# Kernel tuning notes

Measured on AMD Instinct MI355X. Metric: run time of the kernel, lower is better.

The kernel has to match this reference:

```python
import jax, jax.numpy as jnp
import numpy as np

B, T, S, K = 512, 16, 64, 32  # batch, delta_t, num_sensors, num_clusters


def setup_inputs() -> dict:
    key = jax.random.key(0)
    k1, k2, k3 = jax.random.split(key, 3)
    X = jax.random.normal(k1, (B, T, S), dtype=jnp.float32)
    mu = jax.random.normal(k2, (K, S), dtype=jnp.float32)            # cluster means
    A = jax.random.normal(k3, (T, K, S, S), dtype=jnp.float32)       # Toeplitz block generators
    return {"X": X, "mu": mu, "A": A}


def _build_mat(A):
    # A: [T, K, S, S] -> block-Toeplitz mat: [K, T*S, T*S]
    # block(i, j) = A[i-j].T if i >= j else A[j-i]
    T_, K_, S_, _ = A.shape
    idx = jnp.arange(T_)
    diff = idx[:, None] - idx[None, :]                 # [T, T]
    blocks = A[jnp.abs(diff)]                          # [T, T, K, S, S]
    blocks_t = jnp.swapaxes(blocks, -1, -2)
    blocks = jnp.where((diff >= 0)[:, :, None, None, None], blocks_t, blocks)
    # [T, T, K, S, S] -> [K, T, S, T, S] -> [K, T*S, T*S]
    return jnp.transpose(blocks, (2, 0, 3, 1, 4)).reshape(K_, T_ * S_, T_ * S_)


def reference(X, mu, A):
    T_, K_, S_, _ = A.shape
    # dX: [B, K, T, S] -> flatten time*sensor -> [B, K, D]
    dX = (X[:, None, :, :] - mu[None, :, None, :]).reshape(X.shape[0], K_, T_ * S_)
    mat = _build_mat(A)                                # [K, D, D]
    P1 = jnp.einsum('bkd,kde,bke->bk', dX, mat, dX)    # quadratic form
    P2 = jnp.linalg.slogdet(mat)[1]                    # [K] log|det|
    lle = -0.5 * P1 + P2[None, :]
    return jax.nn.softmax(lle, axis=-1)
```

## Files before the change

kernel.cpp:

```cpp
#include <hip/hip_runtime.h>
#include <math.h>

static constexpr int B_ = 512;
static constexpr int T_ = 16;
static constexpr int S_ = 64;
static constexpr int K_ = 32;
static constexpr int N_ = 1024;

__global__ void initk(int* __restrict__ rowmap, float* __restrict__ logdet) {
  int idx = blockIdx.x * 256 + threadIdx.x;
  if (idx < K_ * N_) rowmap[idx] = idx & (N_ - 1);
  if (idx < K_) logdet[idx] = 0.f;
}

__global__ __launch_bounds__(256) void buildM(const float* __restrict__ A, float* __restrict__ M) {
  int k = blockIdx.z, i = blockIdx.y, j = blockIdx.x;
  int d = i - j;
  int ad = d >= 0 ? d : -d;
  const float* Ad = A + ((size_t)(ad * K_ + k) << 12);
  float* out = M + ((size_t)k << 20) + (size_t)(i * 64) * N_ + j * 64;
  int tid = threadIdx.x;
  if (d < 0) {
    for (int x = tid; x < 1024; x += 256) {
      int a = x >> 4, b4 = (x & 15) << 2;
      *(float4*)(out + (size_t)a * N_ + b4) = *(const float4*)(Ad + a * 64 + b4);
    }
  } else {
    __shared__ float ts[64][65];
    for (int x = tid; x < 1024; x += 256) {
      int r = x >> 4, c4 = (x & 15) << 2;
      float4 v = *(const float4*)(Ad + r * 64 + c4);
      ts[c4 + 0][r] = v.x; ts[c4 + 1][r] = v.y; ts[c4 + 2][r] = v.z; ts[c4 + 3][r] = v.w;
    }
    __syncthreads();
    for (int x = tid; x < 1024; x += 256) {
      int a = x >> 4, b4 = (x & 15) << 2;
      float4 v;
      v.x = ts[a][b4 + 0]; v.y = ts[a][b4 + 1]; v.z = ts[a][b4 + 2]; v.w = ts[a][b4 + 3];
      *(float4*)(out + (size_t)a * N_ + b4) = v;
    }
  }
}

__global__ __launch_bounds__(256) void prepk(const float* __restrict__ A, const float* __restrict__ mu,
                                             float* __restrict__ rbuf, float* __restrict__ cterm) {
  int k = blockIdx.x;
  __shared__ float smu[64];
  __shared__ float sp[1024], sq[1024];
  int tid = threadIdx.x;
  if (tid < 64) smu[tid] = mu[k * 64 + tid];
  __syncthreads();
  for (int idx = tid; idx < 1024; idx += 256) {
    int d = idx >> 6, s = idx & 63;
    const float* Ad = A + ((size_t)(d * K_ + k) << 12);
    float ap = 0.f, aq = 0.f;
    for (int s2 = 0; s2 < 64; ++s2) {
      ap += Ad[s * 64 + s2] * smu[s2];
      aq += Ad[s2 * 64 + s] * smu[s2];
    }
    sp[idx] = ap; sq[idx] = aq;
  }
  __syncthreads();
  for (int idx = tid; idx < 1024; idx += 256) {
    int j = idx >> 6, s = idx & 63;
    float acc = 0.5f * (sp[s] + sq[s]);
    for (int d = 1; d < 16; ++d) {
      if (d <= 15 - j) acc += sp[d * 64 + s];
      if (d <= j)      acc += sq[d * 64 + s];
    }
    rbuf[k * 1024 + idx] = acc;
  }
  if (tid < 64) {
    float a = 16.f * sp[tid];
    for (int d = 1; d < 16; ++d) a += 2.f * (float)(16 - d) * sp[d * 64 + tid];
    a *= smu[tid];
    for (int off = 32; off; off >>= 1) a += __shfl_xor(a, off);
    if (tid == 0) cterm[k] = a;
  }
}

__global__ __launch_bounds__(256) void qkern(const float* __restrict__ X, const float* __restrict__ A,
                                             float* __restrict__ Qp) {
  int g = blockIdx.x;
  int btile = blockIdx.y;
  __shared__ float Xs[4][1024];
  __shared__ float Cs[4][4096];
  int tid = threadIdx.x;
  int wave = tid >> 6, lane = tid & 63;
  for (int t = tid; t < 4096; t += 256) {
    int bb = t >> 10, e = t & 1023;
    Xs[bb][e] = X[(size_t)(btile * 4 + bb) * 1024 + e];
  }
  float regQ[4][8];
#pragma unroll
  for (int bb = 0; bb < 4; ++bb)
#pragma unroll
    for (int kk = 0; kk < 8; ++kk) regQ[bb][kk] = 0.f;

  int a0 = (tid >> 4) << 2;
  int v0 = (tid & 15) << 2;
  for (int dd = 0; dd < 4; ++dd) {
    int d = g + (dd << 2);
    __syncthreads();
    for (int bb = 0; bb < 4; ++bb) {
      float4 r0 = {0,0,0,0}, r1 = {0,0,0,0}, r2 = {0,0,0,0}, r3 = {0,0,0,0};
      for (int j = 0; j + d < 16; ++j) {
        const float4 xa = *(const float4*)&Xs[bb][j * 64 + a0];
        const float4 xv = *(const float4*)&Xs[bb][(j + d) * 64 + v0];
        r0.x += xa.x * xv.x; r0.y += xa.x * xv.y; r0.z += xa.x * xv.z; r0.w += xa.x * xv.w;
        r1.x += xa.y * xv.x; r1.y += xa.y * xv.y; r1.z += xa.y * xv.z; r1.w += xa.y * xv.w;
        r2.x += xa.z * xv.x; r2.y += xa.z * xv.y; r2.z += xa.z * xv.z; r2.w += xa.z * xv.w;
        r3.x += xa.w * xv.x; r3.y += xa.w * xv.y; r3.z += xa.w * xv.z; r3.w += xa.w * xv.w;
      }
      *(float4*)&Cs[bb][(a0 + 0) * 64 + v0] = r0;
      *(float4*)&Cs[bb][(a0 + 1) * 64 + v0] = r1;
      *(float4*)&Cs[bb][(a0 + 2) * 64 + v0] = r2;
      *(float4*)&Cs[bb][(a0 + 3) * 64 + v0] = r3;
    }
    __syncthreads();
    float w = (d == 0) ? 1.f : 2.f;
    for (int ch = 0; ch < 16; ++ch) {
      int e4 = (ch * 64 + lane) << 2;
      float4 cv[4];
#pragma unroll
      for (int bb = 0; bb < 4; ++bb) {
        float4 t4 = *(const float4*)&Cs[bb][e4];
        cv[bb].x = w * t4.x; cv[bb].y = w * t4.y; cv[bb].z = w * t4.z; cv[bb].w = w * t4.w;
      }
#pragma unroll
      for (int kk = 0; kk < 8; ++kk) {
        int k = wave + (kk << 2);
        const float4 av = *(const float4*)(A + (((size_t)(d * K_ + k)) << 12) + e4);
#pragma unroll
        for (int bb = 0; bb < 4; ++bb)
          regQ[bb][kk] += av.x * cv[bb].x + av.y * cv[bb].y + av.z * cv[bb].z + av.w * cv[bb].w;
      }
    }
  }
#pragma unroll
  for (int bb = 0; bb < 4; ++bb)
#pragma unroll
    for (int kk = 0; kk < 8; ++kk) {
      float v = regQ[bb][kk];
      for (int off = 32; off; off >>= 1) v += __shfl_xor(v, off);
      regQ[bb][kk] = v;
    }
  if (lane == 0) {
    int b = btile * 4;
#pragma unroll
    for (int bb = 0; bb < 4; ++bb)
#pragma unroll
      for (int kk = 0; kk < 8; ++kk)
        Qp[((size_t)(g * B_ + b + bb) << 5) + (wave + (kk << 2))] = regQ[bb][kk];
  }
}

__global__ __launch_bounds__(1024) void panelk(float* __restrict__ M, int* __restrict__ rowmap,
                                               float* __restrict__ logdet, float* __restrict__ Uws,
                                               int j0) {
  int k = blockIdx.x;
  float* Mk = M + ((size_t)k << 20);
  int* rmk = rowmap + (k << 10);
  int m = N_ - j0;
  int t = threadIdx.x;
  int bdim = blockDim.x;
  int lane = t & 63, wid = t >> 6;
  int nw = (bdim + 63) >> 6;

  __shared__ float bufP[32];
  __shared__ float bufJ[32];
  __shared__ int origP, origJ;
  __shared__ float candv[16];
  __shared__ int candi[16];
  __shared__ int spiv;
  __shared__ float l11s[32 * 33];
  __shared__ int smapU[32];

  float r[32];
  int myorig = -1;
  float mydiag = 1.f;
  bool act = (t < m);
  if (act) {
    myorig = rmk[j0 + t];
    const float* src = Mk + (size_t)myorig * N_ + j0;
#pragma unroll
    for (int c4 = 0; c4 < 8; ++c4) *(float4*)&r[c4 * 4] = *(const float4*)(src + c4 * 4);
  }

#pragma unroll
  for (int jj = 0; jj < 32; ++jj) {
    float bv = (act && t >= jj) ? fabsf(r[jj]) : -1.f;
    int bi = t;
#pragma unroll
    for (int off = 32; off; off >>= 1) {
      float ov = __shfl_xor(bv, off);
      int oi = __shfl_xor(bi, off);
      if (ov > bv) { bv = ov; bi = oi; }
    }
    if (lane == 0) { candv[wid] = bv; candi[wid] = bi; }
    __syncthreads();
    if (t < 64) {
      float cv = (lane < nw) ? candv[lane] : -1.f;
      int ci = (lane < nw) ? candi[lane] : 0;
#pragma unroll
      for (int off = 8; off; off >>= 1) {
        float ov = __shfl_down(cv, off, 16);
        int oi = __shfl_down(ci, off, 16);
        if (ov > cv) { cv = ov; ci = oi; }
      }
      if (lane == 0) spiv = ci;
    }
    __syncthreads();
    int p = spiv;
    if (t == p) {
#pragma unroll
      for (int c4 = 0; c4 < 8; ++c4) *(float4*)&bufP[c4 * 4] = *(const float4*)&r[c4 * 4];
      origP = myorig;
    }
    if (p != jj && t == jj) {
#pragma unroll
      for (int c4 = 0; c4 < 8; ++c4) *(float4*)&bufJ[c4 * 4] = *(const float4*)&r[c4 * 4];
      origJ = myorig;
    }
    __syncthreads();
    float pr[32];
#pragma unroll
    for (int c4 = 0; c4 < 8; ++c4) *(float4*)&pr[c4 * 4] = *(const float4*)&bufP[c4 * 4];
    if (p != jj) {
      if (t == jj) {
#pragma unroll
        for (int c = 0; c < 32; ++c) r[c] = pr[c];
        myorig = origP;
      } else if (t == p) {
#pragma unroll
        for (int c4 = 0; c4 < 8; ++c4) *(float4*)&r[c4 * 4] = *(const float4*)&bufJ[c4 * 4];
        myorig = origJ;
      }
    }
    float pv = pr[jj];
    if (t == jj) mydiag = pv;
    float sinv = 1.0f / pv;
    if (act && t > jj) {
      float mult = r[jj] * sinv;
      r[jj] = mult;
#pragma unroll
      for (int c = jj + 1; c < 32; ++c) r[c] -= mult * pr[c];
    }
  }

  if (t < 32) {
    float lv = logf(fabsf(mydiag));
#pragma unroll
    for (int off = 16; off; off >>= 1) lv += __shfl_down(lv, off, 32);
    if (t == 0) logdet[k] += lv;
  }
  if (t < 32) {
#pragma unroll
    for (int c = 0; c < 32; ++c) l11s[t * 33 + c] = r[c];
    smapU[t] = myorig;
  }
  if (act) {
    float* dst = Mk + (size_t)(j0 + t) * N_ + j0;
#pragma unroll
    for (int c4 = 0; c4 < 8; ++c4) *(float4*)(dst + c4 * 4) = *(const float4*)&r[c4 * 4];
    rmk[j0 + t] = myorig;
  }
  __syncthreads();

  int mprime = m - 32;
  if (t < mprime) {
    int col = j0 + 32 + t;
    float* Uk = Uws + ((size_t)k << 15);
    float u[32];
#pragma unroll
    for (int rr = 0; rr < 32; ++rr) {
      float av = Mk[(size_t)smapU[rr] * N_ + col];
#pragma unroll
      for (int tt = 0; tt < 32; ++tt) { if (tt < rr) av -= l11s[rr * 33 + tt] * u[tt]; }
      u[rr] = av;
      Uk[(rr << 10) + col] = av;
    }
  }
}

__global__ __launch_bounds__(256) void updatek(float* __restrict__ M, const int* __restrict__ rowmap,
                                               const float* __restrict__ Uws, int j0) {
  int k = blockIdx.z;
  int mprime = N_ - j0 - 32;
  int r0 = blockIdx.y << 7;
  int c0 = blockIdx.x << 7;
  float* Mk = M + ((size_t)k << 20);
  const int* rmk = rowmap + (k << 10);
  __shared__ float LtT[32 * 132];
  __shared__ float Ut[32 * 132];
  __shared__ int rowL[128];
  int tid = threadIdx.x;

  if (tid < 128) rowL[tid] = (r0 + tid < mprime) ? rmk[j0 + 32 + r0 + tid] : -1;
  for (int x = tid; x < 1024; x += 256) {
    int rI = x >> 3, q = (x & 7) << 2;
    float4 v = {0.f, 0.f, 0.f, 0.f};
    if (r0 + rI < mprime) v = *(const float4*)(Mk + (size_t)(j0 + 32 + r0 + rI) * N_ + j0 + q);
    LtT[(q + 0) * 132 + rI] = v.x;
    LtT[(q + 1) * 132 + rI] = v.y;
    LtT[(q + 2) * 132 + rI] = v.z;
    LtT[(q + 3) * 132 + rI] = v.w;
  }
  {
    const float* Uk = Uws + ((size_t)k << 15) + j0 + 32 + c0;
    for (int x = tid; x < 1024; x += 256) {
      int rr = x >> 5, c4 = (x & 31) << 2;
      float4 v = {0.f, 0.f, 0.f, 0.f};
      if (c0 + c4 < mprime) v = *(const float4*)(Uk + (rr << 10) + c4);
      *(float4*)&Ut[rr * 132 + c4] = v;
    }
  }
  __syncthreads();

  int tx = tid & 15, ty = tid >> 4;
  int cc = c0 + (tx << 2);

  float4 cur[2][2][4];
#pragma unroll
  for (int ri = 0; ri < 2; ++ri)
#pragma unroll
    for (int r = 0; r < 4; ++r) {
      int lr = (ty << 2) + r + (ri << 6);
      int pr = rowL[lr];
#pragma unroll
      for (int ci = 0; ci < 2; ++ci) {
        int lc = cc + (ci << 6);
        if (pr >= 0 && lc < mprime)
          cur[ri][ci][r] = *(const float4*)(Mk + (size_t)pr * N_ + j0 + 32 + lc);
        else
          cur[ri][ci][r] = make_float4(0.f, 0.f, 0.f, 0.f);
      }
    }

#define FMS4(dst, s, b4) dst.x -= (s) * b4.x; dst.y -= (s) * b4.y; dst.z -= (s) * b4.z; dst.w -= (s) * b4.w;
#pragma unroll 8
  for (int tk = 0; tk < 32; ++tk) {
    float4 aL = *(const float4*)&LtT[tk * 132 + (ty << 2)];
    float4 aH = *(const float4*)&LtT[tk * 132 + (ty << 2) + 64];
    float4 bL = *(const float4*)&Ut[tk * 132 + (tx << 2)];
    float4 bH = *(const float4*)&Ut[tk * 132 + (tx << 2) + 64];
    FMS4(cur[0][0][0], aL.x, bL) FMS4(cur[0][0][1], aL.y, bL) FMS4(cur[0][0][2], aL.z, bL) FMS4(cur[0][0][3], aL.w, bL)
    FMS4(cur[0][1][0], aL.x, bH) FMS4(cur[0][1][1], aL.y, bH) FMS4(cur[0][1][2], aL.z, bH) FMS4(cur[0][1][3], aL.w, bH)
    FMS4(cur[1][0][0], aH.x, bL) FMS4(cur[1][0][1], aH.y, bL) FMS4(cur[1][0][2], aH.z, bL) FMS4(cur[1][0][3], aH.w, bL)
    FMS4(cur[1][1][0], aH.x, bH) FMS4(cur[1][1][1], aH.y, bH) FMS4(cur[1][1][2], aH.z, bH) FMS4(cur[1][1][3], aH.w, bH)
  }
#undef FMS4

#pragma unroll
  for (int ri = 0; ri < 2; ++ri)
#pragma unroll
    for (int r = 0; r < 4; ++r) {
      int lr = (ty << 2) + r + (ri << 6);
      int pr = rowL[lr];
      if (pr < 0) continue;
      float* rowp = Mk + (size_t)pr * N_ + j0 + 32;
#pragma unroll
      for (int ci = 0; ci < 2; ++ci) {
        int lc = cc + (ci << 6);
        if (lc < mprime) *(float4*)(rowp + lc) = cur[ri][ci][r];
      }
    }
}

__global__ __launch_bounds__(256) void finalk(const float* __restrict__ X, const float* __restrict__ rbuf,
                                              const float* __restrict__ cterm, const float* __restrict__ logdet,
                                              const float* __restrict__ Qp, float* __restrict__ out) {
  int b = blockIdx.x;
  __shared__ float Xs[1024];
  __shared__ float lleS[32];
  int tid = threadIdx.x, wave = tid >> 6, lane = tid & 63;
  for (int i = tid; i < 1024; i += 256) Xs[i] = X[(size_t)b * 1024 + i];
  __syncthreads();
#pragma unroll
  for (int kk = 0; kk < 8; ++kk) {
    int k = wave + (kk << 2);
    const float* rk = rbuf + (size_t)k * 1024;
    float acc = 0.f;
#pragma unroll
    for (int ch = 0; ch < 4; ++ch) {
      int e4 = (ch * 64 + lane) << 2;
      const float4 rv = *(const float4*)(rk + e4);
      const float4 xv = *(const float4*)&Xs[e4];
      acc += rv.x * xv.x + rv.y * xv.y + rv.z * xv.z + rv.w * xv.w;
    }
    for (int off = 32; off; off >>= 1) acc += __shfl_xor(acc, off);
    if (lane == 0) {
      float Qv = 0.f;
#pragma unroll
      for (int g = 0; g < 4; ++g) Qv += Qp[((size_t)(g * B_ + b) << 5) + k];
      float P1 = Qv - 2.f * acc + cterm[k];
      lleS[k] = -0.5f * P1 + logdet[k];
    }
  }
  __syncthreads();
  if (wave == 0) {
    float v = lleS[lane & 31];
    float mx = v;
    for (int off = 16; off; off >>= 1) mx = fmaxf(mx, __shfl_xor(mx, off));
    float e = expf(v - mx);
    float s = e;
    for (int off = 16; off; off >>= 1) s += __shfl_xor(s, off);
    if (lane < 32) out[b * 32 + lane] = e / s;
  }
}

extern "C" void kernel_launch(void* const* d_in, const int* in_sizes, int n_in,
                              void* d_out, int out_size, void* d_ws, size_t ws_size,
                              hipStream_t stream) {
  const float* X  = (const float*)d_in[0];
  const float* mu = (const float*)d_in[1];
  const float* A  = (const float*)d_in[2];
  float* out = (float*)d_out;
  float* ws  = (float*)d_ws;

  if (ws_size < 138936576ull) {
    hipMemsetAsync(d_out, 0, (size_t)out_size * sizeof(float), stream);
    return;
  }

  float* M      = ws;
  int*   rowmap = (int*)(ws + 33554432);
  float* logdet = ws + 33587200;
  float* rbuf   = ws + 33587232;
  float* cterm  = ws + 33620000;
  float* Qp     = ws + 33620032;
  float* Uws    = ws + 33685568;

  initk<<<dim3(128), dim3(256), 0, stream>>>(rowmap, logdet);
  buildM<<<dim3(16, 16, 32), dim3(256), 0, stream>>>(A, M);
  prepk<<<dim3(32), dim3(256), 0, stream>>>(A, mu, rbuf, cterm);
  qkern<<<dim3(4, 128), dim3(256), 0, stream>>>(X, A, Qp);

  for (int s = 0; s < 32; ++s) {
    int j0 = s * 32;
    int m = N_ - j0;
    int bt = ((m + 63) >> 6) << 6;
    panelk<<<dim3(32), dim3(bt), 0, stream>>>(M, rowmap, logdet, Uws, j0);
    int mprime = m - 32;
    if (mprime > 0) {
      int mt = (mprime + 127) >> 7;
      updatek<<<dim3(mt, mt, 32), dim3(256), 0, stream>>>(M, rowmap, Uws, j0);
    }
  }

  finalk<<<dim3(512), dim3(256), 0, stream>>>(X, rbuf, cterm, logdet, Qp, out);
}
```

Measured before the change: 2.625 ms.

## Restructure panel LU pivot search to fixed 512 threads with fewer barriers

The panel factorization kernel now runs with a fixed 512 threads, each holding up to two rows in registers, instead of up to 1024 threads with one row each. Pivot selection is reworked so every thread reads the 8 per-wave candidates from shared memory directly, and the next column's candidate search is merged into the end of the current iteration. This cuts the per-column barriers from three to two and drops the single-wave reduction stage. The log-determinant is accumulated by thread 0 as it goes. The cost is doubled register use per thread and, for the first panels, more serial row work per thread.

New measurement: 7.917 ms. 3.02x slower.

```diff
diff --git a/kernel.cpp b/kernel.cpp
--- a/kernel.cpp
+++ b/kernel.cpp
@@ -155,42 +155,46 @@
   }
 }
 
-__global__ __launch_bounds__(1024) void panelk(float* __restrict__ M, int* __restrict__ rowmap,
-                                               float* __restrict__ logdet, float* __restrict__ Uws,
-                                               int j0) {
+__global__ __launch_bounds__(512) void panelk(float* __restrict__ M, int* __restrict__ rowmap,
+                                              float* __restrict__ logdet, float* __restrict__ Uws,
+                                              int j0) {
   int k = blockIdx.x;
   float* Mk = M + ((size_t)k << 20);
   int* rmk = rowmap + (k << 10);
   int m = N_ - j0;
   int t = threadIdx.x;
-  int bdim = blockDim.x;
   int lane = t & 63, wid = t >> 6;
-  int nw = (bdim + 63) >> 6;
 
   __shared__ float bufP[32];
   __shared__ float bufJ[32];
   __shared__ int origP, origJ;
-  __shared__ float candv[16];
-  __shared__ int candi[16];
-  __shared__ int spiv;
+  __shared__ float candv[8];
+  __shared__ int candi[8];
   __shared__ float l11s[32 * 33];
   __shared__ int smapU[32];
 
-  float r[32];
-  int myorig = -1;
-  float mydiag = 1.f;
-  bool act = (t < m);
-  if (act) {
-    myorig = rmk[j0 + t];
-    const float* src = Mk + (size_t)myorig * N_ + j0;
-#pragma unroll
-    for (int c4 = 0; c4 < 8; ++c4) *(float4*)&r[c4 * 4] = *(const float4*)(src + c4 * 4);
-  }
-
-#pragma unroll
-  for (int jj = 0; jj < 32; ++jj) {
-    float bv = (act && t >= jj) ? fabsf(r[jj]) : -1.f;
+  float rA[32], rB[32];
+  int origA = -1, origB = -1;
+  bool actA = (t < m);
+  bool actB = (t + 512 < m);
+  if (actA) {
+    origA = rmk[j0 + t];
+    const float* src = Mk + (size_t)origA * N_ + j0;
+#pragma unroll
+    for (int c4 = 0; c4 < 8; ++c4) *(float4*)&rA[c4 * 4] = *(const float4*)(src + c4 * 4);
+  }
+  if (actB) {
+    origB = rmk[j0 + 512 + t];
+    const float* src = Mk + (size_t)origB * N_ + j0;
+#pragma unroll
+    for (int c4 = 0; c4 < 8; ++c4) *(float4*)&rB[c4 * 4] = *(const float4*)(src + c4 * 4);
+  }
+  float ldacc = 0.f;
+
+  {
+    float bv = actA ? fabsf(rA[0]) : -1.f;
     int bi = t;
+    if (actB) { float v = fabsf(rB[0]); if (v > bv) { bv = v; bi = t + 512; } }
 #pragma unroll
     for (int off = 32; off; off >>= 1) {
       float ov = __shfl_xor(bv, off);
@@ -198,29 +202,29 @@
       if (ov > bv) { bv = ov; bi = oi; }
     }
     if (lane == 0) { candv[wid] = bv; candi[wid] = bi; }
-    __syncthreads();
-    if (t < 64) {
-      float cv = (lane < nw) ? candv[lane] : -1.f;
-      int ci = (lane < nw) ? candi[lane] : 0;
-#pragma unroll
-      for (int off = 8; off; off >>= 1) {
-        float ov = __shfl_down(cv, off, 16);
-        int oi = __shfl_down(ci, off, 16);
-        if (ov > cv) { cv = ov; ci = oi; }
-      }
-      if (lane == 0) spiv = ci;
-    }
-    __syncthreads();
-    int p = spiv;
-    if (t == p) {
-#pragma unroll
-      for (int c4 = 0; c4 < 8; ++c4) *(float4*)&bufP[c4 * 4] = *(const float4*)&r[c4 * 4];
-      origP = myorig;
+  }
+  __syncthreads();
+
+#pragma unroll
+  for (int jj = 0; jj < 32; ++jj) {
+    float cv = candv[0]; int p = candi[0];
+#pragma unroll
+    for (int w = 1; w < 8; ++w) { float v = candv[w]; if (v > cv) { cv = v; p = candi[w]; } }
+    if (p < 512) {
+      if (t == p) {
+#pragma unroll
+        for (int c4 = 0; c4 < 8; ++c4) *(float4*)&bufP[c4 * 4] = *(const float4*)&rA[c4 * 4];
+        origP = origA;
+      }
+    } else if (t == p - 512) {
+#pragma unroll
+      for (int c4 = 0; c4 < 8; ++c4) *(float4*)&bufP[c4 * 4] = *(const float4*)&rB[c4 * 4];
+      origP = origB;
     }
     if (p != jj && t == jj) {
 #pragma unroll
-      for (int c4 = 0; c4 < 8; ++c4) *(float4*)&bufJ[c4 * 4] = *(const float4*)&r[c4 * 4];
-      origJ = myorig;
+      for (int c4 = 0; c4 < 8; ++c4) *(float4*)&bufJ[c4 * 4] = *(const float4*)&rA[c4 * 4];
+      origJ = origA;
     }
     __syncthreads();
     float pr[32];
@@ -229,48 +233,75 @@
     if (p != jj) {
       if (t == jj) {
 #pragma unroll
-        for (int c = 0; c < 32; ++c) r[c] = pr[c];
-        myorig = origP;
-      } else if (t == p) {
-#pragma unroll
-        for (int c4 = 0; c4 < 8; ++c4) *(float4*)&r[c4 * 4] = *(const float4*)&bufJ[c4 * 4];
-        myorig = origJ;
+        for (int c = 0; c < 32; ++c) rA[c] = pr[c];
+        origA = origP;
+      }
+      if (p < 512) {
+        if (t == p) {
+#pragma unroll
+          for (int c4 = 0; c4 < 8; ++c4) *(float4*)&rA[c4 * 4] = *(const float4*)&bufJ[c4 * 4];
+          origA = origJ;
+        }
+      } else if (t == p - 512) {
+#pragma unroll
+        for (int c4 = 0; c4 < 8; ++c4) *(float4*)&rB[c4 * 4] = *(const float4*)&bufJ[c4 * 4];
+        origB = origJ;
       }
     }
     float pv = pr[jj];
-    if (t == jj) mydiag = pv;
+    if (t == 0) ldacc += logf(fabsf(pv));
     float sinv = 1.0f / pv;
-    if (act && t > jj) {
-      float mult = r[jj] * sinv;
-      r[jj] = mult;
-#pragma unroll
-      for (int c = jj + 1; c < 32; ++c) r[c] -= mult * pr[c];
-    }
-  }
-
+    if (actA && t > jj) {
+      float mult = rA[jj] * sinv;
+      rA[jj] = mult;
+#pragma unroll
+      for (int c = jj + 1; c < 32; ++c) rA[c] -= mult * pr[c];
+    }
+    if (actB) {
+      float mult = rB[jj] * sinv;
+      rB[jj] = mult;
+#pragma unroll
+      for (int c = jj + 1; c < 32; ++c) rB[c] -= mult * pr[c];
+    }
+    if (jj < 31) {
+      float bv = (actA && t > jj) ? fabsf(rA[jj + 1]) : -1.f;
+      int bi = t;
+      if (actB) { float v = fabsf(rB[jj + 1]); if (v > bv) { bv = v; bi = t + 512; } }
+#pragma unroll
+      for (int off = 32; off; off >>= 1) {
+        float ov = __shfl_xor(bv, off);
+        int oi = __shfl_xor(bi, off);
+        if (ov > bv) { bv = ov; bi = oi; }
+      }
+      if (lane == 0) { candv[wid] = bv; candi[wid] = bi; }
+    }
+    __syncthreads();
+  }
+
+  if (t == 0) logdet[k] += ldacc;
   if (t < 32) {
-    float lv = logf(fabsf(mydiag));
-#pragma unroll
-    for (int off = 16; off; off >>= 1) lv += __shfl_down(lv, off, 32);
-    if (t == 0) logdet[k] += lv;
-  }
-  if (t < 32) {
-#pragma unroll
-    for (int c = 0; c < 32; ++c) l11s[t * 33 + c] = r[c];
-    smapU[t] = myorig;
-  }
-  if (act) {
+#pragma unroll
+    for (int c = 0; c < 32; ++c) l11s[t * 33 + c] = rA[c];
+    smapU[t] = origA;
+  }
+  if (actA) {
     float* dst = Mk + (size_t)(j0 + t) * N_ + j0;
 #pragma unroll
-    for (int c4 = 0; c4 < 8; ++c4) *(float4*)(dst + c4 * 4) = *(const float4*)&r[c4 * 4];
-    rmk[j0 + t] = myorig;
+    for (int c4 = 0; c4 < 8; ++c4) *(float4*)(dst + c4 * 4) = *(const float4*)&rA[c4 * 4];
+    rmk[j0 + t] = origA;
+  }
+  if (actB) {
+    float* dst = Mk + (size_t)(j0 + 512 + t) * N_ + j0;
+#pragma unroll
+    for (int c4 = 0; c4 < 8; ++c4) *(float4*)(dst + c4 * 4) = *(const float4*)&rB[c4 * 4];
+    rmk[j0 + 512 + t] = origB;
   }
   __syncthreads();
 
   int mprime = m - 32;
-  if (t < mprime) {
-    int col = j0 + 32 + t;
-    float* Uk = Uws + ((size_t)k << 15);
+  float* Uk = Uws + ((size_t)k << 15);
+  for (int cx = t; cx < mprime; cx += 512) {
+    int col = j0 + 32 + cx;
     float u[32];
 #pragma unroll
     for (int rr = 0; rr < 32; ++rr) {
@@ -438,10 +469,8 @@
 
   for (int s = 0; s < 32; ++s) {
     int j0 = s * 32;
-    int m = N_ - j0;
-    int bt = ((m + 63) >> 6) << 6;
-    panelk<<<dim3(32), dim3(bt), 0, stream>>>(M, rowmap, logdet, Uws, j0);
-    int mprime = m - 32;
+    panelk<<<dim3(32), dim3(512), 0, stream>>>(M, rowmap, logdet, Uws, j0);
+    int mprime = N_ - j0 - 32;
     if (mprime > 0) {
       int mt = (mprime + 127) >> 7;
       updatek<<<dim3(mt, mt, 32), dim3(256), 0, stream>>>(M, rowmap, Uws, j0);
```

## Rework LU panel factorization to use LDS slab and deferred row compaction

Applied to the files above, without the earlier changes.

The panel kernel now holds the 1024x32 panel in a padded shared-memory slab with a fixed 512-thread block, each thread owning two rows. It no longer swaps pivot rows; it marks pivot rows as used and compacts the remaining rows at the end. The pivot search is fused into the elimination step, cutting barriers per column from three to two, and the per-thread register array is removed to lower register pressure. In exchange it uses about 150KB of LDS, serialises more of the work per thread, and the variable-bound loops operate on shared memory.

Result: slower. 3.272 ms (+24.6%).

```diff
diff --git a/kernel.cpp b/kernel.cpp
--- a/kernel.cpp
+++ b/kernel.cpp
@@ -155,42 +155,45 @@
   }
 }
 
-__global__ __launch_bounds__(1024) void panelk(float* __restrict__ M, int* __restrict__ rowmap,
-                                               float* __restrict__ logdet, float* __restrict__ Uws,
-                                               int j0) {
+__global__ __launch_bounds__(512, 1) void panelk(float* __restrict__ M, int* __restrict__ rowmap,
+                                                 float* __restrict__ logdet, float* __restrict__ Uws,
+                                                 int j0) {
   int k = blockIdx.x;
   float* Mk = M + ((size_t)k << 20);
   int* rmk = rowmap + (k << 10);
   int m = N_ - j0;
   int t = threadIdx.x;
-  int bdim = blockDim.x;
   int lane = t & 63, wid = t >> 6;
-  int nw = (bdim + 63) >> 6;
-
-  __shared__ float bufP[32];
-  __shared__ float bufJ[32];
-  __shared__ int origP, origJ;
-  __shared__ float candv[16];
-  __shared__ int candi[16];
-  __shared__ int spiv;
-  __shared__ float l11s[32 * 33];
+
+  __shared__ __align__(16) float slab[1024 * 36];
+  __shared__ __align__(16) float l11s[32 * 36];
+  __shared__ __align__(16) float bufP[32];
   __shared__ int smapU[32];
-
-  float r[32];
-  int myorig = -1;
-  float mydiag = 1.f;
-  bool act = (t < m);
-  if (act) {
-    myorig = rmk[j0 + t];
-    const float* src = Mk + (size_t)myorig * N_ + j0;
-#pragma unroll
-    for (int c4 = 0; c4 < 8; ++c4) *(float4*)&r[c4 * 4] = *(const float4*)(src + c4 * 4);
-  }
-
-#pragma unroll
-  for (int jj = 0; jj < 32; ++jj) {
-    float bv = (act && t >= jj) ? fabsf(r[jj]) : -1.f;
+  __shared__ int pivslot[32];
+  __shared__ float candv[8];
+  __shared__ int candi[8];
+
+  int oA = -1, oB = -1;
+  bool aA = (t < m), aB = (t + 512 < m);
+  if (aA) oA = rmk[j0 + t];
+  if (aB) oB = rmk[j0 + 512 + t];
+  if (aA) {
+    const float* src = Mk + (size_t)oA * N_ + j0;
+#pragma unroll
+    for (int c4 = 0; c4 < 8; ++c4) *(float4*)&slab[t * 36 + c4 * 4] = *(const float4*)(src + c4 * 4);
+  }
+  if (aB) {
+    const float* src = Mk + (size_t)oB * N_ + j0;
+#pragma unroll
+    for (int c4 = 0; c4 < 8; ++c4) *(float4*)&slab[(t + 512) * 36 + c4 * 4] = *(const float4*)(src + c4 * 4);
+  }
+  bool uA = false, uB = false;
+  __syncthreads();
+
+  {
+    float bv = aA ? fabsf(slab[t * 36]) : -1.f;
     int bi = t;
+    if (aB) { float v = fabsf(slab[(t + 512) * 36]); if (v > bv) { bv = v; bi = t + 512; } }
 #pragma unroll
     for (int off = 32; off; off >>= 1) {
       float ov = __shfl_xor(bv, off);
@@ -198,85 +201,104 @@
       if (ov > bv) { bv = ov; bi = oi; }
     }
     if (lane == 0) { candv[wid] = bv; candi[wid] = bi; }
+  }
+  __syncthreads();
+
+#pragma unroll 1
+  for (int jj = 0; jj < 32; ++jj) {
+    float cvv = candv[0]; int p = candi[0];
+#pragma unroll
+    for (int w = 1; w < 8; ++w) { float v = candv[w]; if (v > cvv) { cvv = v; p = candi[w]; } }
+    if (t < 32) {
+      float v = slab[p * 36 + t];
+      l11s[jj * 36 + t] = v;
+      bufP[t] = (t > jj) ? v : 0.f;
+    }
+    if (t < 8)
+      *(float4*)(Mk + (size_t)(j0 + jj) * N_ + j0 + t * 4) = *(const float4*)&slab[p * 36 + t * 4];
+    if (t == (p & 511)) {
+      if (p >> 9) { uB = true; smapU[jj] = oB; } else { uA = true; smapU[jj] = oA; }
+      pivslot[jj] = p;
+    }
     __syncthreads();
-    if (t < 64) {
-      float cv = (lane < nw) ? candv[lane] : -1.f;
-      int ci = (lane < nw) ? candi[lane] : 0;
-#pragma unroll
-      for (int off = 8; off; off >>= 1) {
-        float ov = __shfl_down(cv, off, 16);
-        int oi = __shfl_down(ci, off, 16);
-        if (ov > cv) { cv = ov; ci = oi; }
-      }
-      if (lane == 0) spiv = ci;
+    float sinv = 1.0f / l11s[jj * 36 + jj];
+    int g0 = jj >> 2;
+    float bv = -1.f; int bi = t;
+    if (aA && !uA) {
+      int base = t * 36;
+      float mult = slab[base + jj] * sinv;
+      for (int g = g0; g < 8; ++g) {
+        float4 cur = *(const float4*)&slab[base + g * 4];
+        float4 pm = *(const float4*)&bufP[g * 4];
+        cur.x -= mult * pm.x; cur.y -= mult * pm.y; cur.z -= mult * pm.z; cur.w -= mult * pm.w;
+        *(float4*)&slab[base + g * 4] = cur;
+      }
+      slab[base + jj] = mult;
+      if (jj < 31) bv = fabsf(slab[base + jj + 1]);
+    }
+    if (aB && !uB) {
+      int base = (t + 512) * 36;
+      float mult = slab[base + jj] * sinv;
+      for (int g = g0; g < 8; ++g) {
+        float4 cur = *(const float4*)&slab[base + g * 4];
+        float4 pm = *(const float4*)&bufP[g * 4];
+        cur.x -= mult * pm.x; cur.y -= mult * pm.y; cur.z -= mult * pm.z; cur.w -= mult * pm.w;
+        *(float4*)&slab[base + g * 4] = cur;
+      }
+      slab[base + jj] = mult;
+      if (jj < 31) { float v = fabsf(slab[base + jj + 1]); if (v > bv) { bv = v; bi = t + 512; } }
+    }
+    if (jj < 31) {
+#pragma unroll
+      for (int off = 32; off; off >>= 1) {
+        float ov = __shfl_xor(bv, off);
+        int oi = __shfl_xor(bi, off);
+        if (ov > bv) { bv = ov; bi = oi; }
+      }
+      if (lane == 0) { candv[wid] = bv; candi[wid] = bi; }
     }
     __syncthreads();
-    int p = spiv;
-    if (t == p) {
-#pragma unroll
-      for (int c4 = 0; c4 < 8; ++c4) *(float4*)&bufP[c4 * 4] = *(const float4*)&r[c4 * 4];
-      origP = myorig;
-    }
-    if (p != jj && t == jj) {
-#pragma unroll
-      for (int c4 = 0; c4 < 8; ++c4) *(float4*)&bufJ[c4 * 4] = *(const float4*)&r[c4 * 4];
-      origJ = myorig;
-    }
-    __syncthreads();
-    float pr[32];
-#pragma unroll
-    for (int c4 = 0; c4 < 8; ++c4) *(float4*)&pr[c4 * 4] = *(const float4*)&bufP[c4 * 4];
-    if (p != jj) {
-      if (t == jj) {
-#pragma unroll
-        for (int c = 0; c < 32; ++c) r[c] = pr[c];
-        myorig = origP;
-      } else if (t == p) {
-#pragma unroll
-        for (int c4 = 0; c4 < 8; ++c4) *(float4*)&r[c4 * 4] = *(const float4*)&bufJ[c4 * 4];
-        myorig = origJ;
-      }
-    }
-    float pv = pr[jj];
-    if (t == jj) mydiag = pv;
-    float sinv = 1.0f / pv;
-    if (act && t > jj) {
-      float mult = r[jj] * sinv;
-      r[jj] = mult;
-#pragma unroll
-      for (int c = jj + 1; c < 32; ++c) r[c] -= mult * pr[c];
-    }
   }
 
   if (t < 32) {
-    float lv = logf(fabsf(mydiag));
+    float lv = logf(fabsf(l11s[t * 36 + t]));
 #pragma unroll
     for (int off = 16; off; off >>= 1) lv += __shfl_down(lv, off, 32);
     if (t == 0) logdet[k] += lv;
-  }
-  if (t < 32) {
-#pragma unroll
-    for (int c = 0; c < 32; ++c) l11s[t * 33 + c] = r[c];
-    smapU[t] = myorig;
-  }
-  if (act) {
-    float* dst = Mk + (size_t)(j0 + t) * N_ + j0;
-#pragma unroll
-    for (int c4 = 0; c4 < 8; ++c4) *(float4*)(dst + c4 * 4) = *(const float4*)&r[c4 * 4];
-    rmk[j0 + t] = myorig;
-  }
-  __syncthreads();
+    rmk[j0 + t] = smapU[t];
+  }
+  if (aA && !uA) {
+    int cnt = 0;
+#pragma unroll
+    for (int j = 0; j < 32; ++j) cnt += (pivslot[j] < t) ? 1 : 0;
+    int pos = 32 + t - cnt;
+    float* dst = Mk + (size_t)(j0 + pos) * N_ + j0;
+#pragma unroll
+    for (int c4 = 0; c4 < 8; ++c4) *(float4*)(dst + c4 * 4) = *(const float4*)&slab[t * 36 + c4 * 4];
+    rmk[j0 + pos] = oA;
+  }
+  if (aB && !uB) {
+    int g = t + 512;
+    int cnt = 0;
+#pragma unroll
+    for (int j = 0; j < 32; ++j) cnt += (pivslot[j] < g) ? 1 : 0;
+    int pos = 32 + g - cnt;
+    float* dst = Mk + (size_t)(j0 + pos) * N_ + j0;
+#pragma unroll
+    for (int c4 = 0; c4 < 8; ++c4) *(float4*)(dst + c4 * 4) = *(const float4*)&slab[g * 36 + c4 * 4];
+    rmk[j0 + pos] = oB;
+  }
 
   int mprime = m - 32;
-  if (t < mprime) {
-    int col = j0 + 32 + t;
-    float* Uk = Uws + ((size_t)k << 15);
+  float* Uk = Uws + ((size_t)k << 15);
+  for (int cx = t; cx < mprime; cx += 512) {
+    int col = j0 + 32 + cx;
     float u[32];
 #pragma unroll
     for (int rr = 0; rr < 32; ++rr) {
       float av = Mk[(size_t)smapU[rr] * N_ + col];
 #pragma unroll
-      for (int tt = 0; tt < 32; ++tt) { if (tt < rr) av -= l11s[rr * 33 + tt] * u[tt]; }
+      for (int tt = 0; tt < 32; ++tt) { if (tt < rr) av -= l11s[rr * 36 + tt] * u[tt]; }
       u[rr] = av;
       Uk[(rr << 10) + col] = av;
     }
@@ -438,10 +460,8 @@
 
   for (int s = 0; s < 32; ++s) {
     int j0 = s * 32;
-    int m = N_ - j0;
-    int bt = ((m + 63) >> 6) << 6;
-    panelk<<<dim3(32), dim3(bt), 0, stream>>>(M, rowmap, logdet, Uws, j0);
-    int mprime = m - 32;
+    panelk<<<dim3(32), dim3(512), 0, stream>>>(M, rowmap, logdet, Uws, j0);
+    int mprime = N_ - j0 - 32;
     if (mprime > 0) {
       int mt = (mprime + 127) >> 7;
       updatek<<<dim3(mt, mt, 32), dim3(256), 0, stream>>>(M, rowmap, Uws, j0);
```

## Fuse panel triangular solve for U into trailing update kernel

Applied to the files above, without the earlier changes.

Moves the computation of the U block row (forward substitution with L11) out of the single-block-per-matrix panel kernel and into each update block, which now solves its own 128-column slice in shared memory. This removes the Uws workspace round trip and shortens the serial panel step. In exchange, the solve is recomputed redundantly by every row-tile block, and only half the threads do it before the GEMM update.

Result: slower. 2.721 ms (+3.7%).

```diff
diff --git a/kernel.cpp b/kernel.cpp
--- a/kernel.cpp
+++ b/kernel.cpp
@@ -156,8 +156,7 @@
 }
 
 __global__ __launch_bounds__(1024) void panelk(float* __restrict__ M, int* __restrict__ rowmap,
-                                               float* __restrict__ logdet, float* __restrict__ Uws,
-                                               int j0) {
+                                               float* __restrict__ logdet, int j0) {
   int k = blockIdx.x;
   float* Mk = M + ((size_t)k << 20);
   int* rmk = rowmap + (k << 10);
@@ -173,8 +172,6 @@
   __shared__ float candv[16];
   __shared__ int candi[16];
   __shared__ int spiv;
-  __shared__ float l11s[32 * 33];
-  __shared__ int smapU[32];
 
   float r[32];
   int myorig = -1;
@@ -254,49 +251,35 @@
     for (int off = 16; off; off >>= 1) lv += __shfl_down(lv, off, 32);
     if (t == 0) logdet[k] += lv;
   }
-  if (t < 32) {
-#pragma unroll
-    for (int c = 0; c < 32; ++c) l11s[t * 33 + c] = r[c];
-    smapU[t] = myorig;
-  }
   if (act) {
     float* dst = Mk + (size_t)(j0 + t) * N_ + j0;
 #pragma unroll
     for (int c4 = 0; c4 < 8; ++c4) *(float4*)(dst + c4 * 4) = *(const float4*)&r[c4 * 4];
     rmk[j0 + t] = myorig;
   }
-  __syncthreads();
-
-  int mprime = m - 32;
-  if (t < mprime) {
-    int col = j0 + 32 + t;
-    float* Uk = Uws + ((size_t)k << 15);
-    float u[32];
-#pragma unroll
-    for (int rr = 0; rr < 32; ++rr) {
-      float av = Mk[(size_t)smapU[rr] * N_ + col];
-#pragma unroll
-      for (int tt = 0; tt < 32; ++tt) { if (tt < rr) av -= l11s[rr * 33 + tt] * u[tt]; }
-      u[rr] = av;
-      Uk[(rr << 10) + col] = av;
-    }
-  }
 }
 
 __global__ __launch_bounds__(256) void updatek(float* __restrict__ M, const int* __restrict__ rowmap,
-                                               const float* __restrict__ Uws, int j0) {
+                                               int j0) {
   int k = blockIdx.z;
   int mprime = N_ - j0 - 32;
   int r0 = blockIdx.y << 7;
   int c0 = blockIdx.x << 7;
   float* Mk = M + ((size_t)k << 20);
   const int* rmk = rowmap + (k << 10);
+  __shared__ float l11[32 * 36];
   __shared__ float LtT[32 * 132];
   __shared__ float Ut[32 * 132];
   __shared__ int rowL[128];
+  __shared__ int prU[32];
   int tid = threadIdx.x;
 
   if (tid < 128) rowL[tid] = (r0 + tid < mprime) ? rmk[j0 + 32 + r0 + tid] : -1;
+  else if (tid < 160) prU[tid - 128] = rmk[j0 + (tid - 128)];
+  {
+    int rr = tid >> 3, q = (tid & 7) << 2;
+    *(float4*)&l11[rr * 36 + q] = *(const float4*)(Mk + (size_t)(j0 + rr) * N_ + j0 + q);
+  }
   for (int x = tid; x < 1024; x += 256) {
     int rI = x >> 3, q = (x & 7) << 2;
     float4 v = {0.f, 0.f, 0.f, 0.f};
@@ -306,13 +289,19 @@
     LtT[(q + 2) * 132 + rI] = v.z;
     LtT[(q + 3) * 132 + rI] = v.w;
   }
-  {
-    const float* Uk = Uws + ((size_t)k << 15) + j0 + 32 + c0;
-    for (int x = tid; x < 1024; x += 256) {
-      int rr = x >> 5, c4 = (x & 31) << 2;
-      float4 v = {0.f, 0.f, 0.f, 0.f};
-      if (c0 + c4 < mprime) v = *(const float4*)(Uk + (rr << 10) + c4);
-      *(float4*)&Ut[rr * 132 + c4] = v;
+  __syncthreads();
+
+  if (tid < 128) {
+    int c = c0 + tid;
+    bool ok = (c < mprime);
+    float u[32];
+#pragma unroll
+    for (int rr = 0; rr < 32; ++rr) {
+      float av = ok ? Mk[(size_t)prU[rr] * N_ + j0 + 32 + c] : 0.f;
+#pragma unroll
+      for (int tt = 0; tt < 32; ++tt) { if (tt < rr) av -= l11[rr * 36 + tt] * u[tt]; }
+      u[rr] = av;
+      Ut[rr * 132 + tid] = av;
     }
   }
   __syncthreads();
@@ -418,7 +407,7 @@
   float* out = (float*)d_out;
   float* ws  = (float*)d_ws;
 
-  if (ws_size < 138936576ull) {
+  if (ws_size < 134742272ull) {
     hipMemsetAsync(d_out, 0, (size_t)out_size * sizeof(float), stream);
     return;
   }
@@ -429,7 +418,6 @@
   float* rbuf   = ws + 33587232;
   float* cterm  = ws + 33620000;
   float* Qp     = ws + 33620032;
-  float* Uws    = ws + 33685568;
 
   initk<<<dim3(128), dim3(256), 0, stream>>>(rowmap, logdet);
   buildM<<<dim3(16, 16, 32), dim3(256), 0, stream>>>(A, M);
@@ -440,11 +428,11 @@
     int j0 = s * 32;
     int m = N_ - j0;
     int bt = ((m + 63) >> 6) << 6;
-    panelk<<<dim3(32), dim3(bt), 0, stream>>>(M, rowmap, logdet, Uws, j0);
+    panelk<<<dim3(32), dim3(bt), 0, stream>>>(M, rowmap, logdet, j0);
     int mprime = m - 32;
     if (mprime > 0) {
       int mt = (mprime + 127) >> 7;
-      updatek<<<dim3(mt, mt, 32), dim3(256), 0, stream>>>(M, rowmap, Uws, j0);
+      updatek<<<dim3(mt, mt, 32), dim3(256), 0, stream>>>(M, rowmap, j0);
     }
   }
 
```
